# Optimization experiments

Measured on AMD Instinct MI355X. Metric: run time of the kernel, lower is better.

## Reference

```python
import jax, jax.numpy as jnp
import numpy as np

B, D = 8, 256
N_LIVE, K_NEW = 10000, 32
KC = N_LIVE + K_NEW
N_SAMPLES = 100
EPSILON = 0.1


def setup_inputs() -> dict:
    key = jax.random.key(0)
    k1, k2, k3, k4, k5, k6 = jax.random.split(key, 6)
    return {
        "xt": jax.random.normal(k1, (B, D), dtype=jnp.float32),
        "live_x0": jax.random.normal(k2, (B, N_LIVE, D), dtype=jnp.float32),
        "live_ll": jax.random.normal(k3, (B, N_LIVE, 1), dtype=jnp.float32),
        "x0": jax.random.normal(k4, (B, K_NEW, D), dtype=jnp.float32),
        "ll": jax.random.normal(k5, (B, K_NEW, 1), dtype=jnp.float32),
        "t_scale": jnp.float32(0.5),
        "boot_idx": jax.random.randint(k6, (N_SAMPLES, B, KC), 0, KC, dtype=jnp.int32),
    }


def reference(xt, live_x0, live_ll, x0, ll, t_scale, boot_idx):
    # --- spotlight_score core math ---
    # gaussian correction for the new particles: 0.5*||x0-xt||^2/sigma^2 + log(sigma)
    diff_new = x0 - xt[:, None, :]                                   # [B,K,D]
    corr_new = 0.5 * jnp.sum(diff_new ** 2, axis=-1, keepdims=True) / t_scale ** 2  # [B,K,1]
    current_x0 = jnp.concatenate([live_x0, x0], axis=1)              # [B,Kc,D]
    current_ll = jnp.concatenate(
        [live_ll, ll + corr_new + jnp.log(t_scale)], axis=1)         # [B,Kc,1]

    diff = current_x0 - xt[:, None, :]                               # [B,Kc,D]
    use_ll = (current_ll
              - 0.5 * jnp.sum(diff ** 2, axis=-1, keepdims=True) / t_scale ** 2
              - jnp.log(t_scale))                                    # [B,Kc,1]

    scores_p = diff / t_scale                                        # [B,Kc,D] per-particle scores
    logits = use_ll[..., 0]                                          # [B,Kc]

    # --- check_convergence: bootstrap resampled softmax reductions ---
    def body(carry, idx_n):                                          # idx_n: [B,Kc]
        s = jnp.take_along_axis(scores_p, idx_n[:, :, None], axis=1)  # [B,Kc,D]
        l = jnp.take_along_axis(logits, idx_n, axis=1)                # [B,Kc]
        w = jax.nn.softmax(l, axis=1)
        return carry, jnp.einsum('bk,bkd->bd', w, s)                  # [B,D]

    _, boot = jax.lax.scan(body, None, boot_idx)                      # [N,B,D]
    sigma_v = jnp.std(boot, axis=0, ddof=1)                           # [B,D] (torch.std is unbiased)
    converged = jnp.all(sigma_v < EPSILON * t_scale, axis=1)          # [B]

    # --- final importance-weighted score ---
    w = jax.nn.softmax(logits, axis=1)                                # [B,Kc]
    score = jnp.einsum('bk,bkd->bd', w, scores_p)                     # [B,D]
    return score, converged
```

## Files before the change

### kernel.cpp

```cpp
#include <hip/hip_runtime.h>
#include <math.h>

#define B 8
#define D 256
#define N_LIVE 10000
#define K_NEW 32
#define KC 10032
#define NS 100
#define NROW 101
#define EPS 0.1f
#define CAP 1024
#define ACT_CUT 87.0f

#define WS_LOGITS 0
#define WS_ACTE   (WS_LOGITS + B * KC)
#define WS_ACTI   (WS_ACTE + B * CAP)
#define WS_CNT    (WS_ACTI + B * CAP)
#define WS_LUT    (WS_CNT + 8)
#define WS_BOOT   (WS_LUT + B * KC)

__global__ __launch_bounds__(256) void k_logits(
    const float* __restrict__ xt, const float* __restrict__ live_x0,
    const float* __restrict__ live_ll, const float* __restrict__ x0n,
    const float* __restrict__ lln, const float* __restrict__ ts_p,
    float* __restrict__ logits) {
  int b = blockIdx.y;
  int k = blockIdx.x * 4 + (threadIdx.x >> 6);
  int lane = threadIdx.x & 63;
  const float* src = (k < N_LIVE)
      ? (live_x0 + ((size_t)b * N_LIVE + k) * D)
      : (x0n + ((size_t)b * K_NEW + (k - N_LIVE)) * D);
  float4 v = ((const float4*)src)[lane];
  float4 c = ((const float4*)(xt + b * D))[lane];
  float dx = v.x - c.x, dy = v.y - c.y, dz = v.z - c.z, dw = v.w - c.w;
  float s = dx * dx + dy * dy + dz * dz + dw * dw;
#pragma unroll
  for (int off = 32; off; off >>= 1) s += __shfl_xor(s, off);
  if (lane == 0) {
    float ts = *ts_p;
    float out;
    if (k < N_LIVE)
      out = live_ll[(size_t)b * N_LIVE + k] - 0.5f * s / (ts * ts) - logf(ts);
    else
      out = lln[(size_t)b * K_NEW + (k - N_LIVE)];
    logits[(size_t)b * KC + k] = out;
  }
}

__global__ __launch_bounds__(1024) void k_maxsel(
    const float* __restrict__ logits, float* __restrict__ act_e,
    int* __restrict__ act_idx, int* __restrict__ act_cnt, int* __restrict__ lut) {
  int b = blockIdx.x;
  int tid = threadIdx.x;
  const float* lg = logits + (size_t)b * KC;
  __shared__ float smax[16];
  __shared__ int scnt;
  float m = -INFINITY;
  for (int k = tid; k < KC; k += 1024) m = fmaxf(m, lg[k]);
#pragma unroll
  for (int off = 32; off; off >>= 1) m = fmaxf(m, __shfl_xor(m, off));
  if ((tid & 63) == 0) smax[tid >> 6] = m;
  if (tid == 0) scnt = 0;
  __syncthreads();
  float M = smax[0];
#pragma unroll
  for (int i = 1; i < 16; i++) M = fmaxf(M, smax[i]);

  for (int k = tid; k < KC; k += 1024) {
    float l = lg[k];
    int v = 0;
    if (l > M - ACT_CUT) {
      int pos = atomicAdd(&scnt, 1);
      if (pos < CAP) {
        act_e[b * CAP + pos] = expf(l - M);
        act_idx[b * CAP + pos] = k;
        v = pos + 1;
      }
    }
    lut[(size_t)b * KC + k] = v;
  }
  __syncthreads();
  if (tid == 0) act_cnt[b] = min(scnt, CAP);
}

__global__ __launch_bounds__(256) void k_boot(
    const float* __restrict__ live_x0, const float* __restrict__ x0n,
    const float* __restrict__ act_e, const int* __restrict__ act_idx,
    const int* __restrict__ act_cnt, const int* __restrict__ lut,
    const int* __restrict__ boot_idx, float* __restrict__ boot) {
  int n = blockIdx.x;
  int b = blockIdx.y;
  int tid = threadIdx.x;
  __shared__ int cnt[CAP];
  __shared__ float wval[CAP];
  __shared__ int widx[CAP];
  __shared__ int snnz;
  __shared__ float sden[4];
  int A = act_cnt[b];
  for (int i = tid; i < A; i += 256) cnt[i] = 0;
  if (tid == 0) snnz = 0;
  __syncthreads();

  if (n < NS) {
    const int4* row = (const int4*)(boot_idx + ((size_t)n * B + b) * KC);
    const int* lutb = lut + (size_t)b * KC;
    for (int k = tid; k < KC / 4; k += 256) {
      int4 v = row[k];
      int t;
      t = lutb[v.x]; if (t) atomicAdd(&cnt[t - 1], 1);
      t = lutb[v.y]; if (t) atomicAdd(&cnt[t - 1], 1);
      t = lutb[v.z]; if (t) atomicAdd(&cnt[t - 1], 1);
      t = lutb[v.w]; if (t) atomicAdd(&cnt[t - 1], 1);
    }
  } else {
    for (int i = tid; i < A; i += 256) cnt[i] = 1;
  }
  __syncthreads();

  float dpart = 0.f;
  for (int i = tid; i < A; i += 256) {
    int c = cnt[i];
    if (c) {
      float w = (float)c * act_e[b * CAP + i];
      int pos = atomicAdd(&snnz, 1);
      wval[pos] = w;
      widx[pos] = act_idx[b * CAP + i];
      dpart += w;
    }
  }
#pragma unroll
  for (int off = 32; off; off >>= 1) dpart += __shfl_xor(dpart, off);
  if ((tid & 63) == 0) sden[tid >> 6] = dpart;
  __syncthreads();
  float inv = 1.f / (sden[0] + sden[1] + sden[2] + sden[3]);
  int nnz = snnz;

  const float* lx = live_x0 + (size_t)b * N_LIVE * D;
  const float* nx = x0n + (size_t)b * K_NEW * D;
  float acc = 0.f;
  for (int p = 0; p < nnz; p++) {
    int j = widx[p];
    const float* xr = (j < N_LIVE) ? (lx + (size_t)j * D)
                                   : (nx + (size_t)(j - N_LIVE) * D);
    acc = fmaf(wval[p], xr[tid], acc);
  }
  boot[((size_t)b * NROW + n) * D + tid] = acc * inv;
}

__global__ __launch_bounds__(256) void k_final(
    const float* __restrict__ boot, const float* __restrict__ xt,
    const float* __restrict__ ts_p, float* __restrict__ out) {
  int b = blockIdx.x;
  int d = threadIdx.x;
  float ts = *ts_p;
  const float* bb = boot + (size_t)b * NROW * D + d;
  float sum = 0.f;
  for (int n = 0; n < NS; n++) sum += bb[(size_t)n * D];
  float mean = sum / (float)NS;
  float vs = 0.f;
  for (int n = 0; n < NS; n++) { float t = bb[(size_t)n * D] - mean; vs += t * t; }
  float sigma_raw = sqrtf(vs / (float)(NS - 1));
  bool ok = (sigma_raw / ts) < (EPS * ts);
  out[(size_t)b * D + d] = (bb[(size_t)NS * D] - xt[(size_t)b * D + d]) / ts;
  unsigned long long m = __ballot(ok);
  __shared__ int wok[4];
  if ((d & 63) == 0) wok[d >> 6] = (m == 0xFFFFFFFFFFFFFFFFull) ? 1 : 0;
  __syncthreads();
  if (d == 0) out[(size_t)B * D + b] = (wok[0] & wok[1] & wok[2] & wok[3]) ? 1.0f : 0.0f;
}

extern "C" void kernel_launch(void* const* d_in, const int* in_sizes, int n_in,
                              void* d_out, int out_size, void* d_ws, size_t ws_size,
                              hipStream_t stream) {
  const float* xt       = (const float*)d_in[0];
  const float* live_x0  = (const float*)d_in[1];
  const float* live_ll  = (const float*)d_in[2];
  const float* x0n      = (const float*)d_in[3];
  const float* lln      = (const float*)d_in[4];
  const float* ts_p     = (const float*)d_in[5];
  const int*   boot_idx = (const int*)d_in[6];
  float* out = (float*)d_out;
  float* ws  = (float*)d_ws;

  float* logits  = ws + WS_LOGITS;
  float* act_e   = ws + WS_ACTE;
  int*   act_idx = (int*)(ws + WS_ACTI);
  int*   act_cnt = (int*)(ws + WS_CNT);
  int*   lut     = (int*)(ws + WS_LUT);
  float* boot    = ws + WS_BOOT;

  k_logits<<<dim3(KC / 4, B), 256, 0, stream>>>(xt, live_x0, live_ll, x0n, lln, ts_p, logits);
  k_maxsel<<<dim3(B), 1024, 0, stream>>>(logits, act_e, act_idx, act_cnt, lut);
  k_boot<<<dim3(NROW, B), 256, 0, stream>>>(live_x0, x0n, act_e, act_idx, act_cnt, lut, boot_idx, boot);
  k_final<<<dim3(B), 256, 0, stream>>>(boot, xt, ts_p, out);
}
```

Measured before the change: 189.4 us.

## Fuse max into logits kernel, parallelize selection, shrink LUT, unroll gather

```diff
diff --git a/kernel.cpp b/kernel.cpp
--- a/kernel.cpp
+++ b/kernel.cpp
@@ -12,18 +12,26 @@
 #define CAP 1024
 #define ACT_CUT 87.0f
 
-#define WS_LOGITS 0
+#define WS_HDR    0
+#define WS_LOGITS 160
 #define WS_ACTE   (WS_LOGITS + B * KC)
 #define WS_ACTI   (WS_ACTE + B * CAP)
-#define WS_CNT    (WS_ACTI + B * CAP)
-#define WS_LUT    (WS_CNT + 8)
-#define WS_BOOT   (WS_LUT + B * KC)
+#define WS_LUT    (WS_ACTI + B * CAP)
+#define WS_BOOT   (WS_LUT + B * KC / 2)
+
+__device__ __forceinline__ unsigned enc_f32(float f) {
+  unsigned x = __float_as_uint(f);
+  return (x & 0x80000000u) ? ~x : (x | 0x80000000u);
+}
+__device__ __forceinline__ float dec_f32(unsigned k) {
+  return __uint_as_float((k & 0x80000000u) ? (k & 0x7FFFFFFFu) : ~k);
+}
 
 __global__ __launch_bounds__(256) void k_logits(
     const float* __restrict__ xt, const float* __restrict__ live_x0,
     const float* __restrict__ live_ll, const float* __restrict__ x0n,
     const float* __restrict__ lln, const float* __restrict__ ts_p,
-    float* __restrict__ logits) {
+    float* __restrict__ logits, unsigned* __restrict__ hdr) {
   int b = blockIdx.y;
   int k = blockIdx.x * 4 + (threadIdx.x >> 6);
   int lane = threadIdx.x & 63;
@@ -36,6 +44,7 @@
   float s = dx * dx + dy * dy + dz * dz + dw * dw;
 #pragma unroll
   for (int off = 32; off; off >>= 1) s += __shfl_xor(s, off);
+  __shared__ float wlog[4];
   if (lane == 0) {
     float ts = *ts_p;
     float out;
@@ -44,49 +53,43 @@
     else
       out = lln[(size_t)b * K_NEW + (k - N_LIVE)];
     logits[(size_t)b * KC + k] = out;
-  }
-}
-
-__global__ __launch_bounds__(1024) void k_maxsel(
-    const float* __restrict__ logits, float* __restrict__ act_e,
-    int* __restrict__ act_idx, int* __restrict__ act_cnt, int* __restrict__ lut) {
-  int b = blockIdx.x;
-  int tid = threadIdx.x;
+    wlog[threadIdx.x >> 6] = out;
+  }
+  __syncthreads();
+  if (threadIdx.x == 0) {
+    float m = fmaxf(fmaxf(wlog[0], wlog[1]), fmaxf(wlog[2], wlog[3]));
+    atomicMax(&hdr[b * 16], enc_f32(m));
+  }
+}
+
+__global__ __launch_bounds__(256) void k_select(
+    const float* __restrict__ logits, unsigned* __restrict__ hdr,
+    float* __restrict__ act_e, int* __restrict__ act_idx,
+    unsigned short* __restrict__ lut) {
+  int b = blockIdx.y;
+  int tid = blockIdx.x * 256 + threadIdx.x;
+  float M = dec_f32(hdr[b * 16]);
   const float* lg = logits + (size_t)b * KC;
-  __shared__ float smax[16];
-  __shared__ int scnt;
-  float m = -INFINITY;
-  for (int k = tid; k < KC; k += 1024) m = fmaxf(m, lg[k]);
-#pragma unroll
-  for (int off = 32; off; off >>= 1) m = fmaxf(m, __shfl_xor(m, off));
-  if ((tid & 63) == 0) smax[tid >> 6] = m;
-  if (tid == 0) scnt = 0;
-  __syncthreads();
-  float M = smax[0];
-#pragma unroll
-  for (int i = 1; i < 16; i++) M = fmaxf(M, smax[i]);
-
-  for (int k = tid; k < KC; k += 1024) {
+  int* cnt = (int*)&hdr[128 + b];
+  for (int k = tid; k < KC; k += 8 * 256) {
     float l = lg[k];
-    int v = 0;
+    unsigned short v = 0;
     if (l > M - ACT_CUT) {
-      int pos = atomicAdd(&scnt, 1);
+      int pos = atomicAdd(cnt, 1);
       if (pos < CAP) {
         act_e[b * CAP + pos] = expf(l - M);
         act_idx[b * CAP + pos] = k;
-        v = pos + 1;
+        v = (unsigned short)(pos + 1);
       }
     }
     lut[(size_t)b * KC + k] = v;
   }
-  __syncthreads();
-  if (tid == 0) act_cnt[b] = min(scnt, CAP);
 }
 
 __global__ __launch_bounds__(256) void k_boot(
     const float* __restrict__ live_x0, const float* __restrict__ x0n,
     const float* __restrict__ act_e, const int* __restrict__ act_idx,
-    const int* __restrict__ act_cnt, const int* __restrict__ lut,
+    const unsigned* __restrict__ hdr, const unsigned short* __restrict__ lut,
     const int* __restrict__ boot_idx, float* __restrict__ boot) {
   int n = blockIdx.x;
   int b = blockIdx.y;
@@ -96,14 +99,14 @@
   __shared__ int widx[CAP];
   __shared__ int snnz;
   __shared__ float sden[4];
-  int A = act_cnt[b];
+  int A = min((int)hdr[128 + b], CAP);
   for (int i = tid; i < A; i += 256) cnt[i] = 0;
   if (tid == 0) snnz = 0;
   __syncthreads();
 
   if (n < NS) {
     const int4* row = (const int4*)(boot_idx + ((size_t)n * B + b) * KC);
-    const int* lutb = lut + (size_t)b * KC;
+    const unsigned short* lutb = lut + (size_t)b * KC;
     for (int k = tid; k < KC / 4; k += 256) {
       int4 v = row[k];
       int t;
@@ -137,14 +140,22 @@
 
   const float* lx = live_x0 + (size_t)b * N_LIVE * D;
   const float* nx = x0n + (size_t)b * K_NEW * D;
-  float acc = 0.f;
-  for (int p = 0; p < nnz; p++) {
+  float acc0 = 0.f, acc1 = 0.f;
+  int p = 0;
+  for (; p + 1 < nnz; p += 2) {
+    int j0 = widx[p], j1 = widx[p + 1];
+    const float* r0 = (j0 < N_LIVE) ? (lx + (size_t)j0 * D) : (nx + (size_t)(j0 - N_LIVE) * D);
+    const float* r1 = (j1 < N_LIVE) ? (lx + (size_t)j1 * D) : (nx + (size_t)(j1 - N_LIVE) * D);
+    float x0v = r0[tid], x1v = r1[tid];
+    acc0 = fmaf(wval[p], x0v, acc0);
+    acc1 = fmaf(wval[p + 1], x1v, acc1);
+  }
+  if (p < nnz) {
     int j = widx[p];
-    const float* xr = (j < N_LIVE) ? (lx + (size_t)j * D)
-                                   : (nx + (size_t)(j - N_LIVE) * D);
-    acc = fmaf(wval[p], xr[tid], acc);
-  }
-  boot[((size_t)b * NROW + n) * D + tid] = acc * inv;
+    const float* xr = (j < N_LIVE) ? (lx + (size_t)j * D) : (nx + (size_t)(j - N_LIVE) * D);
+    acc0 = fmaf(wval[p], xr[tid], acc0);
+  }
+  boot[((size_t)b * NROW + n) * D + tid] = (acc0 + acc1) * inv;
 }
 
 __global__ __launch_bounds__(256) void k_final(
@@ -182,15 +193,17 @@
   float* out = (float*)d_out;
   float* ws  = (float*)d_ws;
 
-  float* logits  = ws + WS_LOGITS;
-  float* act_e   = ws + WS_ACTE;
-  int*   act_idx = (int*)(ws + WS_ACTI);
-  int*   act_cnt = (int*)(ws + WS_CNT);
-  int*   lut     = (int*)(ws + WS_LUT);
-  float* boot    = ws + WS_BOOT;
-
-  k_logits<<<dim3(KC / 4, B), 256, 0, stream>>>(xt, live_x0, live_ll, x0n, lln, ts_p, logits);
-  k_maxsel<<<dim3(B), 1024, 0, stream>>>(logits, act_e, act_idx, act_cnt, lut);
-  k_boot<<<dim3(NROW, B), 256, 0, stream>>>(live_x0, x0n, act_e, act_idx, act_cnt, lut, boot_idx, boot);
+  unsigned* hdr            = (unsigned*)(ws + WS_HDR);
+  float* logits            = ws + WS_LOGITS;
+  float* act_e             = ws + WS_ACTE;
+  int*   act_idx           = (int*)(ws + WS_ACTI);
+  unsigned short* lut      = (unsigned short*)(ws + WS_LUT);
+  float* boot              = ws + WS_BOOT;
+
+  hipMemsetAsync(hdr, 0, 160 * sizeof(unsigned), stream);
+
+  k_logits<<<dim3(KC / 4, B), 256, 0, stream>>>(xt, live_x0, live_ll, x0n, lln, ts_p, logits, hdr);
+  k_select<<<dim3(8, B), 256, 0, stream>>>(logits, hdr, act_e, act_idx, lut);
+  k_boot<<<dim3(NROW, B), 256, 0, stream>>>(live_x0, x0n, act_e, act_idx, hdr, lut, boot_idx, boot);
   k_final<<<dim3(B), 256, 0, stream>>>(boot, xt, ts_p, out);
 }
```

Result: slower. 259.0 us (+36.8%).
